# Kernel optimization log

Measured on AMD Instinct MI355X. Metric: run time of the kernel, lower is better.

Reference implementation:

```python
import jax, jax.numpy as jnp
import numpy as np
import math

B, S, D = 2, 2048, 1024
H = 16
HD = D // H          # 64
ROT = HD             # rotary_pct = 1.0 -> full head dim
BASE = 10000.0


def _rotate_half(x):
    half = x.shape[-1] // 2
    return jnp.concatenate([-x[..., half:], x[..., :half]], axis=-1)


def _cos_sin(seq_len, dtype):
    inv_freq = 1.0 / (BASE ** (jnp.arange(0, ROT, 2, dtype=jnp.float32) / ROT))
    t = jnp.arange(seq_len, dtype=jnp.float32)
    freqs = jnp.einsum('i,j->ij', t, inv_freq)            # [S, ROT/2]
    emb = jnp.concatenate([freqs, freqs], axis=-1)        # [S, ROT]
    return jnp.cos(emb).astype(dtype)[None, None], jnp.sin(emb).astype(dtype)[None, None]


def setup_inputs() -> dict:
    key = jax.random.key(0)
    k1, k2, k3 = jax.random.split(key, 3)
    x = jax.random.normal(k1, (B, S, D), dtype=jnp.float32)
    attn_mask = jnp.ones((B, S), dtype=jnp.int32)
    W_qkv = jax.random.normal(k2, (3 * D, D), dtype=jnp.float32) * 0.02
    W_out = jax.random.normal(k3, (D, D), dtype=jnp.float32) * 0.02
    return {"x": x, "attn_mask": attn_mask, "W_qkv": W_qkv, "W_out": W_out}


def reference(x, attn_mask, W_qkv, W_out):
    bsz, seq_len, _ = x.shape
    dtype = x.dtype
    neg = jnp.finfo(dtype).min

    qkv = jnp.einsum('bsd,ed->bse', x, W_qkv)                     # [B,S,3D]
    qkv = qkv.reshape(bsz, seq_len, 3, H, HD).transpose(2, 0, 3, 1, 4)
    q, k, v = qkv[0], qkv[1], qkv[2]                              # [B,H,S,HD]

    cos, sin = _cos_sin(seq_len, dtype)                           # [1,1,S,ROT]
    q = q * cos + _rotate_half(q) * sin
    k = k * cos + _rotate_half(k) * sin

    scores = jnp.einsum('bhqd,bhkd->bhqk', q, k) / math.sqrt(HD)  # [B,H,S,S]
    causal = jnp.tril(jnp.ones((seq_len, seq_len), dtype=bool))
    scores = jnp.where(causal[None, None], scores, neg)
    # 2D padding mask over key positions
    scores = jnp.where((attn_mask[:, None, None, :] == 0), neg, scores)

    attn = jax.nn.softmax(scores, axis=-1)
    out = jnp.einsum('bhqk,bhkd->bhqd', attn, v)                  # [B,H,S,HD]
    out = out.transpose(0, 2, 1, 3).reshape(bsz, seq_len, D)
    return jnp.einsum('bsd,ed->bse', out, W_out)
```

## Files before the change

### kernel.cpp

```cpp
#include <hip/hip_runtime.h>
#include <hip/hip_bf16.h>
#include <math.h>
#include <stdint.h>

typedef __hip_bfloat16 bf16;
typedef __attribute__((ext_vector_type(8))) short short8;
typedef __attribute__((ext_vector_type(4))) float f32x4;
typedef __attribute__((ext_vector_type(16))) float f32x16;

#define NB 2
#define NS 2048
#define ND 1024
#define NH 16
#define NHD 64
#define N3D 3072

#define SM_SCALE 0.18033688011112042f

__device__ __forceinline__ void gload16(const bf16* g, void* l) {
  __builtin_amdgcn_global_load_lds(
      (const __attribute__((address_space(1))) uint32_t*)g,
      (__attribute__((address_space(3))) uint32_t*)l, 16, 0, 0);
}

__global__ void cast3_kernel(const float4* __restrict__ x, bf16* __restrict__ xb,
                             const float4* __restrict__ wq, bf16* __restrict__ wqb,
                             const float4* __restrict__ wo, bf16* __restrict__ wob) {
  int i = blockIdx.x * blockDim.x + threadIdx.x;
  const float4* src;
  bf16* dst;
  int off;
  if (i < 1048576) {
    src = x; dst = xb; off = i;
  } else if (i < 1835008) {
    src = wq; dst = wqb; off = i - 1048576;
  } else {
    src = wo; dst = wob; off = i - 1835008;
  }
  float4 v = src[off];
  alignas(8) bf16 r[4];
  r[0] = __float2bfloat16(v.x);
  r[1] = __float2bfloat16(v.y);
  r[2] = __float2bfloat16(v.z);
  r[3] = __float2bfloat16(v.w);
  *reinterpret_cast<uint2*>(dst + (size_t)off * 4) = *reinterpret_cast<const uint2*>(r);
}

__global__ void ropetab_kernel(float* __restrict__ cs_tab, float* __restrict__ sn_tab) {
  int idx = blockIdx.x * blockDim.x + threadIdx.x;
  int j = idx & 31;
  int s = idx >> 5;
  float inv = exp2f((float)(2 * j) * (-13.287712379549449f / 64.0f));
  float ang = (float)s * inv;
  float sn, cs;
  sincosf(ang, &sn, &cs);
  cs_tab[idx] = cs;
  sn_tab[idx] = sn;
}

__global__ __launch_bounds__(512) void gemm_qkv(const bf16* __restrict__ Ap,
                                                const bf16* __restrict__ Bp,
                                                const float* __restrict__ cs_tab,
                                                const float* __restrict__ sn_tab,
                                                bf16* __restrict__ Qr, bf16* __restrict__ Kr,
                                                bf16* __restrict__ Vt) {
  __shared__ short L[2][32768];
  const int tid = threadIdx.x;
  const int lane = tid & 63;
  const int w = tid >> 6;
  const int wm = w >> 2, wn = w & 3;
  const int l15 = lane & 15, l4 = lane >> 4;
  const int lin = blockIdx.x;
  const int xcd = lin & 7, t2 = lin >> 3;
  const int byy = (xcd << 2) | (t2 & 3);
  const int g = t2 >> 2;
  const int bm0 = byy * 128;
  const int bn0 = g * 128;

  const int rw = lane >> 3, sg = lane & 7;
  const int swseg = (sg ^ rw) * 8;
  const int reg = w >> 1;
  const int rowb = (w & 1) * 64 + rw;
  const bf16* srcbase;
  if (reg == 0)
    srcbase = Ap + (size_t)(bm0 + rowb) * 1024 + swseg;
  else
    srcbase = Bp + (size_t)((reg - 1) * 1024 + bn0 + rowb) * 1024 + swseg;
  const int ldsb = w * 4096;

  f32x4 acc[3][4][2] = {};

  auto issue = [&](int t) {
    short* dst = &L[t & 1][ldsb];
    const bf16* s = srcbase + t * 64;
#pragma unroll
    for (int j = 0; j < 8; ++j) gload16(s + (size_t)j * 8 * 1024, dst + j * 512);
  };

  issue(0);
  asm volatile("s_waitcnt vmcnt(0)" ::: "memory");
  __builtin_amdgcn_s_barrier();

  for (int t = 0; t < 16; ++t) {
    const short* S = L[t & 1];
    if (t + 1 < 16) issue(t + 1);
#pragma unroll
    for (int kk = 0; kk < 2; ++kk) {
      short8 af[4];
#pragma unroll
      for (int mi = 0; mi < 4; ++mi) {
        int row = wm * 64 + mi * 16 + l15;
        af[mi] = *(const short8*)&S[row * 64 + (((kk * 4 + l4) ^ (row & 7)) << 3)];
      }
#pragma unroll
      for (int tt = 0; tt < 3; ++tt) {
        short8 bfr[2];
#pragma unroll
        for (int ni = 0; ni < 2; ++ni) {
          int row = (wn >> 1) * 64 + (wn & 1) * 16 + ni * 32 + l15;
          bfr[ni] = *(const short8*)&S[(1 + tt) * 8192 + row * 64 +
                                       (((kk * 4 + l4) ^ (row & 7)) << 3)];
        }
        __builtin_amdgcn_s_setprio(1);
#pragma unroll
        for (int mi = 0; mi < 4; ++mi)
#pragma unroll
          for (int ni = 0; ni < 2; ++ni)
            acc[tt][mi][ni] = __builtin_amdgcn_mfma_f32_16x16x32_bf16(
                af[mi], bfr[ni], acc[tt][mi][ni], 0, 0, 0);
        __builtin_amdgcn_s_setprio(0);
      }
    }
    if (t + 1 < 16) {
      asm volatile("s_waitcnt vmcnt(0)" ::: "memory");
      __builtin_amdgcn_s_barrier();
    }
  }

  {
    const int j = (wn & 1) * 16 + l15;
    const int hq = g * 2 + (wn >> 1);
#pragma unroll
    for (int tt = 0; tt < 2; ++tt) {
      bf16* dst = tt ? Kr : Qr;
#pragma unroll
      for (int mi = 0; mi < 4; ++mi)
#pragma unroll
        for (int r = 0; r < 4; ++r) {
          int row = bm0 + wm * 64 + mi * 16 + l4 * 4 + r;
          int b = row >> 11;
          int s = row & (NS - 1);
          float cs = cs_tab[s * 32 + j];
          float sn = sn_tab[s * 32 + j];
          float v0 = acc[tt][mi][0][r];
          float v1 = acc[tt][mi][1][r];
          size_t base = ((size_t)(b * NH + hq) * NS + s) * NHD + j;
          dst[base] = __float2bfloat16(v0 * cs - v1 * sn);
          dst[base + 32] = __float2bfloat16(v1 * cs + v0 * sn);
        }
    }
  }
  __syncthreads();
  {
    bf16* vtile = reinterpret_cast<bf16*>(&L[0][0]);
#pragma unroll
    for (int mi = 0; mi < 4; ++mi)
#pragma unroll
      for (int ni = 0; ni < 2; ++ni)
#pragma unroll
        for (int r = 0; r < 4; ++r) {
          int srow = wm * 64 + mi * 16 + l4 * 4 + r;
          int c = (wn >> 1) * 64 + (wn & 1) * 16 + ni * 32 + l15;
          vtile[c * 136 + srow] = __float2bfloat16(acc[2][mi][ni][r]);
        }
    __syncthreads();
    const int b_ = bm0 >> 11;
    const int s0 = (bm0 & (NS - 1)) + (tid & 3) * 32;
    const int c = tid >> 2;
    const int head = g * 2 + (c >> 6);
    bf16* dstp = Vt + (((size_t)(b_ * NH + head)) * NHD + (c & 63)) * NS + s0;
#pragma unroll
    for (int gg = 0; gg < 4; ++gg)
      *reinterpret_cast<short8*>(dstp + gg * 8) =
          *reinterpret_cast<const short8*>(&vtile[c * 136 + (tid & 3) * 32 + gg * 8]);
  }
}

#define GEMM_PIPE_BODY(...)                                                               \
  __shared__ short As[3][128 * 64];                                                       \
  __shared__ short Bs[3][128 * 64];                                                       \
  const int tid = threadIdx.x;                                                            \
  const int lane = tid & 63;                                                              \
  const int w = tid >> 6;                                                                 \
  const int wm = w >> 2, wn = w & 3;                                                      \
  const int l15 = lane & 15, l4 = lane >> 4;                                              \
  const int r0 = tid >> 3, seg = tid & 7;                                                 \
  const int sw = ((seg ^ (r0 & 7)) << 3);                                                 \
  const bf16* Ar0 = Ap + (size_t)(bm0 + r0) * 1024 + sw;                                  \
  const bf16* Ar1 = Ap + (size_t)(bm0 + r0 + 64) * 1024 + sw;                             \
  const bf16* Br0 = Bp + (size_t)(bn0 + r0) * 1024 + sw;                                  \
  const bf16* Br1 = Bp + (size_t)(bn0 + r0 + 64) * 1024 + sw;                             \
  f32x4 acc[4][2] = {};                                                                   \
  gload16(Ar0 + 0, &As[0][w * 512]);                                                      \
  gload16(Ar1 + 0, &As[0][4096 + w * 512]);                                               \
  gload16(Br0 + 0, &Bs[0][w * 512]);                                                      \
  gload16(Br1 + 0, &Bs[0][4096 + w * 512]);                                               \
  gload16(Ar0 + 64, &As[1][w * 512]);                                                     \
  gload16(Ar1 + 64, &As[1][4096 + w * 512]);                                              \
  gload16(Br0 + 64, &Bs[1][w * 512]);                                                     \
  gload16(Br1 + 64, &Bs[1][4096 + w * 512]);                                              \
  asm volatile("s_waitcnt vmcnt(4)" ::: "memory");                                        \
  __builtin_amdgcn_s_barrier();                                                           \
  for (int t = 0; t < 16; ++t) {                                                          \
    const int slot = t % 3;                                                               \
    if (t + 2 < 16) {                                                                     \
      const int ns = (t + 2) % 3;                                                         \
      const int nk = (t + 2) * 64;                                                        \
      gload16(Ar0 + nk, &As[ns][w * 512]);                                                \
      gload16(Ar1 + nk, &As[ns][4096 + w * 512]);                                         \
      gload16(Br0 + nk, &Bs[ns][w * 512]);                                                \
      gload16(Br1 + nk, &Bs[ns][4096 + w * 512]);                                         \
    }                                                                                     \
    _Pragma("unroll") for (int kk = 0; kk < 2; ++kk) {                                    \
      short8 af[4], bfr[2];                                                               \
      _Pragma("unroll") for (int mi = 0; mi < 4; ++mi) {                                  \
        int row = wm * 64 + mi * 16 + l15;                                                \
        af[mi] = *(const short8*)&As[slot][row * 64 + (((kk * 4 + l4) ^ (row & 7)) << 3)];\
      }                                                                                   \
      _Pragma("unroll") for (int ni = 0; ni < 2; ++ni) {                                  \
        int row = (wn >> 1) * 64 + (wn & 1) * 16 + ni * 32 + l15;                         \
        bfr[ni] = *(const short8*)&Bs[slot][row * 64 + (((kk * 4 + l4) ^ (row & 7)) << 3)];\
      }                                                                                   \
      __builtin_amdgcn_s_setprio(1);                                                      \
      _Pragma("unroll") for (int mi = 0; mi < 4; ++mi)                                    \
        _Pragma("unroll") for (int ni = 0; ni < 2; ++ni)                                  \
          acc[mi][ni] =                                                                   \
              __builtin_amdgcn_mfma_f32_16x16x32_bf16(af[mi], bfr[ni], acc[mi][ni], 0, 0, 0);\
      __builtin_amdgcn_s_setprio(0);                                                      \
    }                                                                                     \
    if (t + 2 < 16) {                                                                     \
      asm volatile("s_waitcnt vmcnt(4)" ::: "memory");                                    \
      __builtin_amdgcn_s_barrier();                                                       \
    } else if (t < 15) {                                                                  \
      asm volatile("s_waitcnt vmcnt(0)" ::: "memory");                                    \
      __builtin_amdgcn_s_barrier();                                                       \
    }                                                                                     \
  }                                                                                       \
  __VA_ARGS__

__global__ __launch_bounds__(512) void gemm_bt(const bf16* __restrict__ Ap,
                                               const bf16* __restrict__ Bp,
                                               float* __restrict__ Cv) {
  const int lin = blockIdx.x;
  const int xcd = lin & 7, idx = lin >> 3;
  const int bxx = (xcd & 1) * 4 + (idx & 3);
  const int byy = (xcd >> 1) * 8 + (idx >> 2);
  const int bn0 = bxx * 128, bm0 = byy * 128;
  GEMM_PIPE_BODY(
    _Pragma("unroll") for (int mi = 0; mi < 4; ++mi) {
      _Pragma("unroll") for (int ni = 0; ni < 2; ++ni) {
        _Pragma("unroll") for (int r = 0; r < 4; ++r) {
          int row = bm0 + wm * 64 + mi * 16 + l4 * 4 + r;
          int col = bn0 + (wn >> 1) * 64 + (wn & 1) * 16 + ni * 32 + l15;
          Cv[(size_t)row * ND + col] = acc[mi][ni][r];
        }
      }
    }
  )
}

__global__ void maskbias_kernel(const int* __restrict__ amask, float* __restrict__ mb, int n) {
  int i = blockIdx.x * blockDim.x + threadIdx.x;
  if (i < n) mb[i] = amask[i] ? 0.f : -1e30f;
}

__global__ __launch_bounds__(256, 2) void attn_kernel(const bf16* __restrict__ Qr,
                                                      const bf16* __restrict__ Kr,
                                                      const bf16* __restrict__ Vt,
                                                      const float* __restrict__ mb,
                                                      bf16* __restrict__ AO) {
  __shared__ short Ks[2][64 * 64];
  __shared__ short Vs[2][64 * 64];
  __shared__ float Mb[2][64];

  const int tid = threadIdx.x;
  const int lane = tid & 63;
  const int w = tid >> 6;
  const int q = lane & 31;
  const int hi = lane >> 5;

  const int lin = blockIdx.x;
  const int xcd = lin & 7;
  const int k = lin >> 3;
  const int bh = xcd * 4 + (k & 3);
  const int kk = k >> 2;
  const int tile = (k < 32) ? (15 - kk) : (kk - 8);
  const int b = bh >> 4, h = bh & 15;
  const int qw = tile * 128 + w * 32;
  const int nc = 2 * tile + 2;

  const bf16* Qb = Qr + (size_t)bh * NS * NHD;
  const bf16* Kb = Kr + (size_t)bh * NS * NHD;
  const bf16* Vb = Vt + (size_t)bh * NHD * NS;

  const int srow = tid >> 2;
  const int sc0 = (tid & 3) * 16;
  const int swz = (srow & 7) << 3;

  short8 Qf[4];
#pragma unroll
  for (int s = 0; s < 4; ++s)
    Qf[s] = *reinterpret_cast<const short8*>(&Qb[(size_t)(qw + q) * NHD + s * 16 + hi * 8]);

  f32x16 o0 = {}, o1 = {};
  float mx = -1e30f, lsum = 0.f;

  short8 kreg[2], vreg[2];
  float4 mreg;
  auto prefetch = [&](int kv0) {
    kreg[0] = *reinterpret_cast<const short8*>(&Kb[(size_t)(kv0 + srow) * NHD + sc0]);
    kreg[1] = *reinterpret_cast<const short8*>(&Kb[(size_t)(kv0 + srow) * NHD + sc0 + 8]);
    vreg[0] = *reinterpret_cast<const short8*>(&Vb[(size_t)srow * NS + kv0 + sc0]);
    vreg[1] = *reinterpret_cast<const short8*>(&Vb[(size_t)srow * NS + kv0 + sc0 + 8]);
    if (tid < 16) mreg = *reinterpret_cast<const float4*>(&mb[b * NS + kv0 + tid * 4]);
  };
  auto stage = [&](int buf) {
    *reinterpret_cast<short8*>(&Ks[buf][srow * 64 + (sc0 ^ swz)]) = kreg[0];
    *reinterpret_cast<short8*>(&Ks[buf][srow * 64 + ((sc0 + 8) ^ swz)]) = kreg[1];
    *reinterpret_cast<short8*>(&Vs[buf][srow * 64 + (sc0 ^ swz)]) = vreg[0];
    *reinterpret_cast<short8*>(&Vs[buf][srow * 64 + ((sc0 + 8) ^ swz)]) = vreg[1];
    if (tid < 16) *reinterpret_cast<float4*>(&Mb[buf][tid * 4]) = mreg;
  };

  prefetch(0);
  stage(0);
  __syncthreads();

  const int rsw = (q & 7) << 3;

  for (int c = 0; c < nc; ++c) {
    const int cur = c & 1;
    const int kv0 = c * 64;
    if (c + 1 < nc) prefetch((c + 1) * 64);

    if (kv0 < qw + 32) {
      f32x16 a0 = {}, a1 = {};
#pragma unroll
      for (int s = 0; s < 4; ++s) {
        short8 kf0 = *reinterpret_cast<const short8*>(
            &Ks[cur][q * 64 + ((s * 16 + hi * 8) ^ rsw)]);
        short8 kf1 = *reinterpret_cast<const short8*>(
            &Ks[cur][(32 + q) * 64 + ((s * 16 + hi * 8) ^ rsw)]);
        a0 = __builtin_amdgcn_mfma_f32_32x32x16_bf16(kf0, Qf[s], a0, 0, 0, 0);
        a1 = __builtin_amdgcn_mfma_f32_32x32x16_bf16(kf1, Qf[s], a1, 0, 0, 0);
      }

      float4 bv[2][4];
#pragma unroll
      for (int t = 0; t < 2; ++t)
#pragma unroll
        for (int g = 0; g < 4; ++g)
          bv[t][g] = *reinterpret_cast<const float4*>(&Mb[cur][t * 32 + g * 8 + hi * 4]);
      const int qg = qw + q;
#pragma unroll
      for (int t = 0; t < 2; ++t) {
        f32x16& a = t ? a1 : a0;
        const bool needc = (kv0 + t * 32 + 31 > qw);
#pragma unroll
        for (int r = 0; r < 16; ++r) {
          float v = fmaf(a[r], SM_SCALE, ((const float*)&bv[t][r >> 2])[r & 3]);
          if (needc) {
            int kvg = kv0 + t * 32 + (r & 3) + 8 * (r >> 2) + 4 * hi;
            if (kvg > qg) v = -1e30f;
          }
          a[r] = v;
        }
      }

      float cm = a0[0];
#pragma unroll
      for (int r = 1; r < 16; ++r) cm = fmaxf(cm, a0[r]);
#pragma unroll
      for (int r = 0; r < 16; ++r) cm = fmaxf(cm, a1[r]);
      float pm = fmaxf(cm, __shfl_xor(cm, 32));

      if (!__all(pm <= mx + 8.f)) {
        float mn = fmaxf(mx, pm);
        float fac = __builtin_amdgcn_exp2f(mx - mn);
        mx = mn;
        lsum *= fac;
#pragma unroll
        for (int r = 0; r < 16; ++r) {
          float fq = __shfl(fac, (r & 3) + 8 * (r >> 2) + 4 * hi);
          o0[r] *= fq;
          o1[r] *= fq;
        }
      }

      float rs = 0.f;
      short8 pa[4];
#pragma unroll
      for (int t = 0; t < 2; ++t) {
        f32x16& a = t ? a1 : a0;
#pragma unroll
        for (int r = 0; r < 16; ++r) {
          float e = __builtin_amdgcn_exp2f(a[r] - mx);
          a[r] = e;
          rs += e;
        }
#pragma unroll
        for (int g = 0; g < 2; ++g) {
          union { unsigned int u; __hip_bfloat162 h2; } X, X2, Y, Y2;
          X.h2 = __float22bfloat162_rn(float2{a[g * 8 + 0], a[g * 8 + 1]});
          X2.h2 = __float22bfloat162_rn(float2{a[g * 8 + 2], a[g * 8 + 3]});
          Y.h2 = __float22bfloat162_rn(float2{a[g * 8 + 4], a[g * 8 + 5]});
          Y2.h2 = __float22bfloat162_rn(float2{a[g * 8 + 6], a[g * 8 + 7]});
          asm volatile("v_permlane32_swap_b32 %0, %1" : "+v"(X.u), "+v"(Y.u));
          asm volatile("v_permlane32_swap_b32 %0, %1" : "+v"(X2.u), "+v"(Y2.u));
          union { unsigned int u[4]; short8 s; } P;
          P.u[0] = X.u;
          P.u[1] = X2.u;
          P.u[2] = Y.u;
          P.u[3] = Y2.u;
          pa[t * 2 + g] = P.s;
        }
      }
      lsum += rs + __shfl_xor(rs, 32);

#pragma unroll
      for (int ks = 0; ks < 4; ++ks) {
        const int vcol = (ks * 16 + hi * 8) ^ rsw;
        short8 vf0 = *reinterpret_cast<const short8*>(&Vs[cur][q * 64 + vcol]);
        short8 vf1 = *reinterpret_cast<const short8*>(&Vs[cur][(32 + q) * 64 + vcol]);
        o0 = __builtin_amdgcn_mfma_f32_32x32x16_bf16(pa[ks], vf0, o0, 0, 0, 0);
        o1 = __builtin_amdgcn_mfma_f32_32x32x16_bf16(pa[ks], vf1, o1, 0, 0, 0);
      }
    }

    if (c + 1 < nc) stage(cur ^ 1);
    __syncthreads();
  }

  float inv = 1.0f / lsum;
#pragma unroll
  for (int r = 0; r < 16; ++r) {
    const int crow = (r & 3) + 8 * (r >> 2) + 4 * hi;
    float iq = __shfl(inv, crow);
    size_t base = (size_t)(b * NS + qw + crow) * ND + h * NHD;
    AO[base + q] = __float2bfloat16(o0[r] * iq);
    AO[base + 32 + q] = __float2bfloat16(o1[r] * iq);
  }
}

extern "C" void kernel_launch(void* const* d_in, const int* in_sizes, int n_in,
                              void* d_out, int out_size, void* d_ws, size_t ws_size,
                              hipStream_t stream) {
  const float* x = (const float*)d_in[0];
  const int* amask = (const int*)d_in[1];
  const float* Wqkv = (const float*)d_in[2];
  const float* Wout = (const float*)d_in[3];
  float* out = (float*)d_out;

  char* p = (char*)d_ws;
  bf16* xb = (bf16*)(p);
  bf16* wqkvb = (bf16*)(p + 8388608);
  bf16* woutb = (bf16*)(p + 14680064);
  float* cs_tab = (float*)(p + 25165824);
  float* sn_tab = (float*)(p + 25427968);
  float* mbias = (float*)(p + 25690112);
  bf16* Qr = (bf16*)(p + 41943040);
  bf16* Kr = (bf16*)(p + 50331648);
  bf16* Vt = (bf16*)(p + 58720256);
  bf16* AO = xb;

  cast3_kernel<<<8192, 256, 0, stream>>>((const float4*)x, xb, (const float4*)Wqkv, wqkvb,
                                         (const float4*)Wout, woutb);
  ropetab_kernel<<<256, 256, 0, stream>>>(cs_tab, sn_tab);

  gemm_qkv<<<256, 512, 0, stream>>>(xb, wqkvb, cs_tab, sn_tab, Qr, Kr, Vt);
  maskbias_kernel<<<16, 256, 0, stream>>>(amask, mbias, NB * NS);
  attn_kernel<<<512, 256, 0, stream>>>(Qr, Kr, Vt, mbias, AO);
  gemm_bt<<<256, 512, 0, stream>>>(AO, woutb, out);
}
```

Measured before the change: 120.3 us.

## Split long causal attention tiles across two blocks with a combine pass

For query tiles 8–15, the KV loop is split into two halves, each handled by its own block, which writes unnormalized fp32 partial outputs plus running max and sum. A new combine kernel merges the halves with log-sum-exp rescaling and writes bf16 output. A slot table reorders work so the grid grows from 512 to 768 blocks with more even per-block work, reducing the causal load-imbalance tail. The cost is extra partial-output traffic, an additional kernel launch, and a workspace region reused for the partials that overlaps the rope tables.

Result: faster. 116.3 us (-3.4%).

```diff
diff --git a/kernel.cpp b/kernel.cpp
--- a/kernel.cpp
+++ b/kernel.cpp
@@ -16,6 +16,12 @@
 #define N3D 3072
 
 #define SM_SCALE 0.18033688011112042f
+
+__constant__ const unsigned char SLOT_TILE[24] = {15, 15, 7, 14, 14, 13, 13, 6,
+                                                  12, 12, 11, 11, 5, 10, 10, 9,
+                                                  9,  4,  8,  8,  3, 2,  1,  0};
+__constant__ const unsigned char SLOT_MODE[24] = {1, 2, 0, 1, 2, 1, 2, 0, 1, 2, 1, 2,
+                                                  0, 1, 2, 1, 2, 0, 1, 2, 0, 0, 0, 0};
 
 __device__ __forceinline__ void gload16(const bf16* g, void* l) {
   __builtin_amdgcn_global_load_lds(
@@ -278,7 +284,9 @@
                                                       const bf16* __restrict__ Kr,
                                                       const bf16* __restrict__ Vt,
                                                       const float* __restrict__ mb,
-                                                      bf16* __restrict__ AO) {
+                                                      bf16* __restrict__ AO,
+                                                      float* __restrict__ Opart,
+                                                      float2* __restrict__ ML) {
   __shared__ short Ks[2][64 * 64];
   __shared__ short Vs[2][64 * 64];
   __shared__ float Mb[2][64];
@@ -293,11 +301,13 @@
   const int xcd = lin & 7;
   const int k = lin >> 3;
   const int bh = xcd * 4 + (k & 3);
-  const int kk = k >> 2;
-  const int tile = (k < 32) ? (15 - kk) : (kk - 8);
+  const int slot = k >> 2;
+  const int tile = SLOT_TILE[slot];
+  const int mode = SLOT_MODE[slot];
   const int b = bh >> 4, h = bh & 15;
   const int qw = tile * 128 + w * 32;
-  const int nc = 2 * tile + 2;
+  const int c0 = (mode == 2) ? tile + 1 : 0;
+  const int c1 = (mode == 1) ? tile + 1 : 2 * tile + 2;
 
   const bf16* Qb = Qr + (size_t)bh * NS * NHD;
   const bf16* Kb = Kr + (size_t)bh * NS * NHD;
@@ -332,16 +342,16 @@
     if (tid < 16) *reinterpret_cast<float4*>(&Mb[buf][tid * 4]) = mreg;
   };
 
-  prefetch(0);
+  prefetch(c0 * 64);
   stage(0);
   __syncthreads();
 
   const int rsw = (q & 7) << 3;
 
-  for (int c = 0; c < nc; ++c) {
-    const int cur = c & 1;
+  for (int c = c0; c < c1; ++c) {
+    const int cur = (c - c0) & 1;
     const int kv0 = c * 64;
-    if (c + 1 < nc) prefetch((c + 1) * 64);
+    if (c + 1 < c1) prefetch((c + 1) * 64);
 
     if (kv0 < qw + 32) {
       f32x16 a0 = {}, a1 = {};
@@ -437,18 +447,69 @@
       }
     }
 
-    if (c + 1 < nc) stage(cur ^ 1);
+    if (c + 1 < c1) stage(cur ^ 1);
     __syncthreads();
   }
 
-  float inv = 1.0f / lsum;
-#pragma unroll
-  for (int r = 0; r < 16; ++r) {
-    const int crow = (r & 3) + 8 * (r >> 2) + 4 * hi;
-    float iq = __shfl(inv, crow);
-    size_t base = (size_t)(b * NS + qw + crow) * ND + h * NHD;
-    AO[base + q] = __float2bfloat16(o0[r] * iq);
-    AO[base + 32 + q] = __float2bfloat16(o1[r] * iq);
+  if (mode == 0) {
+    float inv = 1.0f / lsum;
+#pragma unroll
+    for (int r = 0; r < 16; ++r) {
+      const int crow = (r & 3) + 8 * (r >> 2) + 4 * hi;
+      float iq = __shfl(inv, crow);
+      size_t base = (size_t)(b * NS + qw + crow) * ND + h * NHD;
+      AO[base + q] = __float2bfloat16(o0[r] * iq);
+      AO[base + 32 + q] = __float2bfloat16(o1[r] * iq);
+    }
+  } else {
+    const int ps = (tile - 8) * 2 + (mode - 1);
+    float* Ob = Opart + ((size_t)(ps * 32 + bh) * 128) * 64;
+    if (hi == 0) ML[(ps * 32 + bh) * 128 + w * 32 + q] = float2{mx, lsum};
+#pragma unroll
+    for (int r = 0; r < 16; ++r) {
+      const int crow = (r & 3) + 8 * (r >> 2) + 4 * hi;
+      Ob[(w * 32 + crow) * 64 + q] = o0[r];
+      Ob[(w * 32 + crow) * 64 + 32 + q] = o1[r];
+    }
+  }
+}
+
+__global__ __launch_bounds__(256) void combine_kernel(const float* __restrict__ Opart,
+                                                      const float2* __restrict__ ML,
+                                                      bf16* __restrict__ AO) {
+  const int unit = blockIdx.x;
+  const int t8 = unit >> 5, bh = unit & 31;
+  const int tile = 8 + t8;
+  const int b = bh >> 4, h = bh & 15;
+  const int ps0 = t8 * 2, ps1 = t8 * 2 + 1;
+  const int row = threadIdx.x >> 1;
+  const int ch = (threadIdx.x & 1) * 32;
+  float2 ml0 = ML[(ps0 * 32 + bh) * 128 + row];
+  float2 ml1 = ML[(ps1 * 32 + bh) * 128 + row];
+  float m = fmaxf(ml0.x, ml1.x);
+  float s0 = exp2f(ml0.x - m), s1 = exp2f(ml1.x - m);
+  float invl = 1.0f / (ml0.y * s0 + ml1.y * s1);
+  s0 *= invl;
+  s1 *= invl;
+  const float* O0 = Opart + ((size_t)(ps0 * 32 + bh) * 128 + row) * 64 + ch;
+  const float* O1 = Opart + ((size_t)(ps1 * 32 + bh) * 128 + row) * 64 + ch;
+  bf16* dst = AO + (size_t)(b * NS + tile * 128 + row) * ND + h * NHD + ch;
+#pragma unroll
+  for (int g = 0; g < 4; ++g) {
+    float4 a0 = *reinterpret_cast<const float4*>(O0 + g * 8);
+    float4 a1 = *reinterpret_cast<const float4*>(O0 + g * 8 + 4);
+    float4 c0 = *reinterpret_cast<const float4*>(O1 + g * 8);
+    float4 c1 = *reinterpret_cast<const float4*>(O1 + g * 8 + 4);
+    alignas(16) bf16 rr[8];
+    rr[0] = __float2bfloat16(a0.x * s0 + c0.x * s1);
+    rr[1] = __float2bfloat16(a0.y * s0 + c0.y * s1);
+    rr[2] = __float2bfloat16(a0.z * s0 + c0.z * s1);
+    rr[3] = __float2bfloat16(a0.w * s0 + c0.w * s1);
+    rr[4] = __float2bfloat16(a1.x * s0 + c1.x * s1);
+    rr[5] = __float2bfloat16(a1.y * s0 + c1.y * s1);
+    rr[6] = __float2bfloat16(a1.z * s0 + c1.z * s1);
+    rr[7] = __float2bfloat16(a1.w * s0 + c1.w * s1);
+    *reinterpret_cast<short8*>(dst + g * 8) = *reinterpret_cast<const short8*>(rr);
   }
 }
 
@@ -465,9 +526,11 @@
   bf16* xb = (bf16*)(p);
   bf16* wqkvb = (bf16*)(p + 8388608);
   bf16* woutb = (bf16*)(p + 14680064);
+  float* mbias = (float*)(p + 16777216);
+  float2* ML = (float2*)(p + 16793600);
   float* cs_tab = (float*)(p + 25165824);
   float* sn_tab = (float*)(p + 25427968);
-  float* mbias = (float*)(p + 25690112);
+  float* Opart = (float*)(p + 25165824);
   bf16* Qr = (bf16*)(p + 41943040);
   bf16* Kr = (bf16*)(p + 50331648);
   bf16* Vt = (bf16*)(p + 58720256);
@@ -479,6 +542,7 @@
 
   gemm_qkv<<<256, 512, 0, stream>>>(xb, wqkvb, cs_tab, sn_tab, Qr, Kr, Vt);
   maskbias_kernel<<<16, 256, 0, stream>>>(amask, mbias, NB * NS);
-  attn_kernel<<<512, 256, 0, stream>>>(Qr, Kr, Vt, mbias, AO);
+  attn_kernel<<<768, 256, 0, stream>>>(Qr, Kr, Vt, mbias, AO, Opart, ML);
+  combine_kernel<<<256, 256, 0, stream>>>(Opart, ML, AO);
   gemm_bt<<<256, 512, 0, stream>>>(AO, woutb, out);
 }
```

## Split long causal attention tiles across KV chunks and merge with combine kernel

Applied to the files above, without the earlier changes.

Query tiles with many KV chunks are now split into up to four partial blocks, using constant schedule tables. Each partial block writes a normalized partial output plus its running max and sum, and a new combine kernel merges them with log-sum-exp weights. The grid grows from 512 to 1280 blocks so that causal work is spread more evenly across CUs and the long-tile tail is shortened. In exchange it adds an extra kernel launch, partial-output traffic through workspace memory, and bf16 rounding of the partial results; mbias is also moved into reused workspace space.

Result: slower. 129.5 us (+7.7%).

```diff
diff --git a/kernel.cpp b/kernel.cpp
--- a/kernel.cpp
+++ b/kernel.cpp
@@ -16,6 +16,25 @@
 #define N3D 3072
 
 #define SM_SCALE 0.18033688011112042f
+
+__constant__ const unsigned char S_TILE[40] = {3, 7, 7, 10, 11, 11, 11, 14, 14, 15,
+                                               15, 15, 15, 6, 6, 9, 9, 10, 10, 12,
+                                               12, 13, 13, 13, 13, 14, 14, 2, 5, 5,
+                                               8, 8, 8, 9, 12, 12, 4, 4, 1, 0};
+__constant__ const unsigned char S_C0[40] = {0, 0, 8, 0, 0, 8, 16, 0, 8, 0,
+                                             8, 16, 24, 0, 7, 0, 7, 8, 15, 0,
+                                             7, 0, 7, 14, 21, 16, 23, 0, 0, 6,
+                                             0, 6, 12, 14, 14, 20, 0, 5, 0, 0};
+__constant__ const unsigned char S_C1[40] = {8, 8, 16, 8, 8, 16, 24, 8, 16, 8,
+                                             16, 24, 32, 7, 14, 7, 14, 15, 22, 7,
+                                             14, 7, 14, 21, 28, 23, 30, 6, 6, 12,
+                                             6, 12, 18, 20, 20, 26, 5, 10, 4, 2};
+__constant__ const unsigned char S_PS[40] = {255, 6, 7, 14, 17, 18, 19, 28, 29, 32,
+                                             33, 34, 35, 4, 5, 11, 12, 15, 16, 20,
+                                             21, 24, 25, 26, 27, 30, 31, 255, 2, 3,
+                                             8, 9, 10, 13, 22, 23, 0, 1, 255, 255};
+__constant__ const unsigned char PS_BASE[16] = {0, 0, 0, 0, 0, 2, 4, 6, 8, 11, 14, 17, 20, 24, 28, 32};
+__constant__ const unsigned char NP_TAB[16] = {1, 1, 1, 1, 2, 2, 2, 2, 3, 3, 3, 3, 4, 4, 4, 4};
 
 __device__ __forceinline__ void gload16(const bf16* g, void* l) {
   __builtin_amdgcn_global_load_lds(
@@ -278,7 +297,9 @@
                                                       const bf16* __restrict__ Kr,
                                                       const bf16* __restrict__ Vt,
                                                       const float* __restrict__ mb,
-                                                      bf16* __restrict__ AO) {
+                                                      bf16* __restrict__ AO,
+                                                      bf16* __restrict__ Opart,
+                                                      float2* __restrict__ ML) {
   __shared__ short Ks[2][64 * 64];
   __shared__ short Vs[2][64 * 64];
   __shared__ float Mb[2][64];
@@ -293,11 +314,13 @@
   const int xcd = lin & 7;
   const int k = lin >> 3;
   const int bh = xcd * 4 + (k & 3);
-  const int kk = k >> 2;
-  const int tile = (k < 32) ? (15 - kk) : (kk - 8);
+  const int slot = k >> 2;
+  const int tile = S_TILE[slot];
+  const int c0 = S_C0[slot];
+  const int c1 = S_C1[slot];
+  const int ps = S_PS[slot];
   const int b = bh >> 4, h = bh & 15;
   const int qw = tile * 128 + w * 32;
-  const int nc = 2 * tile + 2;
 
   const bf16* Qb = Qr + (size_t)bh * NS * NHD;
   const bf16* Kb = Kr + (size_t)bh * NS * NHD;
@@ -332,16 +355,16 @@
     if (tid < 16) *reinterpret_cast<float4*>(&Mb[buf][tid * 4]) = mreg;
   };
 
-  prefetch(0);
+  prefetch(c0 * 64);
   stage(0);
   __syncthreads();
 
   const int rsw = (q & 7) << 3;
 
-  for (int c = 0; c < nc; ++c) {
-    const int cur = c & 1;
+  for (int c = c0; c < c1; ++c) {
+    const int cur = (c - c0) & 1;
     const int kv0 = c * 64;
-    if (c + 1 < nc) prefetch((c + 1) * 64);
+    if (c + 1 < c1) prefetch((c + 1) * 64);
 
     if (kv0 < qw + 32) {
       f32x16 a0 = {}, a1 = {};
@@ -437,18 +460,80 @@
       }
     }
 
-    if (c + 1 < nc) stage(cur ^ 1);
+    if (c + 1 < c1) stage(cur ^ 1);
     __syncthreads();
   }
 
   float inv = 1.0f / lsum;
-#pragma unroll
-  for (int r = 0; r < 16; ++r) {
-    const int crow = (r & 3) + 8 * (r >> 2) + 4 * hi;
-    float iq = __shfl(inv, crow);
-    size_t base = (size_t)(b * NS + qw + crow) * ND + h * NHD;
-    AO[base + q] = __float2bfloat16(o0[r] * iq);
-    AO[base + 32 + q] = __float2bfloat16(o1[r] * iq);
+  if (ps == 255) {
+#pragma unroll
+    for (int r = 0; r < 16; ++r) {
+      const int crow = (r & 3) + 8 * (r >> 2) + 4 * hi;
+      float iq = __shfl(inv, crow);
+      size_t base = (size_t)(b * NS + qw + crow) * ND + h * NHD;
+      AO[base + q] = __float2bfloat16(o0[r] * iq);
+      AO[base + 32 + q] = __float2bfloat16(o1[r] * iq);
+    }
+  } else {
+    bf16* Ob = Opart + ((size_t)(ps * 32 + bh) * 128) * 64;
+    if (hi == 0) ML[(ps * 32 + bh) * 128 + w * 32 + q] = float2{mx, lsum};
+#pragma unroll
+    for (int r = 0; r < 16; ++r) {
+      const int crow = (r & 3) + 8 * (r >> 2) + 4 * hi;
+      float iq = __shfl(inv, crow);
+      Ob[(w * 32 + crow) * 64 + q] = __float2bfloat16(o0[r] * iq);
+      Ob[(w * 32 + crow) * 64 + 32 + q] = __float2bfloat16(o1[r] * iq);
+    }
+  }
+}
+
+__global__ __launch_bounds__(256) void combine_kernel(const bf16* __restrict__ Opart,
+                                                      const float2* __restrict__ ML,
+                                                      bf16* __restrict__ AO) {
+  const int bx = blockIdx.x;
+  const int tile = 4 + (bx >> 5);
+  const int bh = bx & 31;
+  const int b = bh >> 4, h = bh & 15;
+  const int np = NP_TAB[tile];
+  const int pb = PS_BASE[tile];
+  const int row = threadIdx.x >> 1;
+  const int ch = (threadIdx.x & 1) * 32;
+
+  float mm = -1e30f;
+  float2 ml[4];
+  for (int i = 0; i < np; ++i) {
+    ml[i] = ML[((pb + i) * 32 + bh) * 128 + row];
+    mm = fmaxf(mm, ml[i].x);
+  }
+  float wgt[4];
+  float wsum = 0.f;
+  for (int i = 0; i < np; ++i) {
+    wgt[i] = ml[i].y * exp2f(ml[i].x - mm);
+    wsum += wgt[i];
+  }
+  float invw = 1.0f / wsum;
+
+  float acc[32] = {};
+  for (int i = 0; i < np; ++i) {
+    const bf16* Op = Opart + ((size_t)((pb + i) * 32 + bh) * 128 + row) * 64 + ch;
+    float wi = wgt[i] * invw;
+#pragma unroll
+    for (int g = 0; g < 4; ++g) {
+      short8 v = *reinterpret_cast<const short8*>(Op + g * 8);
+#pragma unroll
+      for (int e = 0; e < 8; ++e) {
+        unsigned int u = ((unsigned int)(unsigned short)v[e]) << 16;
+        acc[g * 8 + e] += wi * __uint_as_float(u);
+      }
+    }
+  }
+  bf16* dst = AO + (size_t)(b * NS + tile * 128 + row) * ND + h * NHD + ch;
+#pragma unroll
+  for (int g = 0; g < 4; ++g) {
+    alignas(16) bf16 rr[8];
+#pragma unroll
+    for (int e = 0; e < 8; ++e) rr[e] = __float2bfloat16(acc[g * 8 + e]);
+    *reinterpret_cast<short8*>(dst + g * 8) = *reinterpret_cast<const short8*>(rr);
   }
 }
 
@@ -464,10 +549,12 @@
   char* p = (char*)d_ws;
   bf16* xb = (bf16*)(p);
   bf16* wqkvb = (bf16*)(p + 8388608);
+  float* mbias = (float*)(p + 8388608);
+  float2* ML = (float2*)(p + 8404992);
   bf16* woutb = (bf16*)(p + 14680064);
+  bf16* Opart = (bf16*)(p + 16777216);
   float* cs_tab = (float*)(p + 25165824);
   float* sn_tab = (float*)(p + 25427968);
-  float* mbias = (float*)(p + 25690112);
   bf16* Qr = (bf16*)(p + 41943040);
   bf16* Kr = (bf16*)(p + 50331648);
   bf16* Vt = (bf16*)(p + 58720256);
@@ -479,6 +566,7 @@
 
   gemm_qkv<<<256, 512, 0, stream>>>(xb, wqkvb, cs_tab, sn_tab, Qr, Kr, Vt);
   maskbias_kernel<<<16, 256, 0, stream>>>(amask, mbias, NB * NS);
-  attn_kernel<<<512, 256, 0, stream>>>(Qr, Kr, Vt, mbias, AO);
+  attn_kernel<<<1280, 256, 0, stream>>>(Qr, Kr, Vt, mbias, AO, Opart, ML);
+  combine_kernel<<<384, 256, 0, stream>>>(Opart, ML, AO);
   gemm_bt<<<256, 512, 0, stream>>>(AO, woutb, out);
 }
```
